# Kernel tuning notes

Measured on AMD Instinct MI355X. Metric: run time of the kernel, lower is better.

Reference implementation:

```python
import jax, jax.numpy as jnp
import numpy as np

D_MODEL = 2048
N_HEADS = 16
HEAD_DIM = D_MODEL // N_HEADS


def setup_inputs() -> dict:
    key = jax.random.key(0)
    ks = jax.random.split(key, 9)
    s = 0.02
    B, S = 4, 2048
    return {
        "x": jax.random.normal(ks[0], (B, S, D_MODEL), dtype=jnp.float32),
        "Wq": jax.random.normal(ks[1], (D_MODEL, D_MODEL), dtype=jnp.float32) * s,
        "bq": jnp.zeros((D_MODEL,), dtype=jnp.float32),
        "Wk": jax.random.normal(ks[2], (D_MODEL, D_MODEL), dtype=jnp.float32) * s,
        "bk": jnp.zeros((D_MODEL,), dtype=jnp.float32),
        "Wv": jax.random.normal(ks[3], (D_MODEL, D_MODEL), dtype=jnp.float32) * s,
        "bv": jnp.zeros((D_MODEL,), dtype=jnp.float32),
        "Wo": jax.random.normal(ks[4], (D_MODEL, D_MODEL), dtype=jnp.float32) * s,
        "bo": jnp.zeros((D_MODEL,), dtype=jnp.float32),
    }


def reference(x, Wq, bq, Wk, bk, Wv, bv, Wo, bo):
    B, S, _ = x.shape
    scale = jnp.asarray(np.sqrt(HEAD_DIM), dtype=x.dtype)

    def split_heads(t):  # [B,S,D] -> [B,H,S,hd]
        return t.reshape(B, S, N_HEADS, HEAD_DIM).transpose(0, 2, 1, 3)

    q = split_heads(x @ Wq + bq)
    k = split_heads(x @ Wk + bk)
    v = split_heads(x @ Wv + bv)

    # scores: [B,H,S,S]
    attn = jnp.einsum('bhqd,bhkd->bhqk', q, k) / scale
    kv_len = S
    causal = jnp.triu(jnp.ones((S, kv_len), dtype=bool), k=kv_len - S + 1)
    attn = jnp.where(causal[None, None], -jnp.inf, attn)
    attn = jax.nn.softmax(attn, axis=-1)
    # dropout is identity (p=0 / eval mode)
    out = jnp.einsum('bhqk,bhkd->bhqd', attn, v)
    out = out.transpose(0, 2, 1, 3).reshape(B, S, D_MODEL)
    return out @ Wo + bo
```

## Files before the change

### kernel.cpp

```cpp
#include <hip/hip_runtime.h>
#include <hip/hip_bf16.h>

#define DEV __device__ __forceinline__

typedef __bf16 bf16_t;
typedef __bf16 bf16x8 __attribute__((ext_vector_type(8)));
typedef __bf16 bf16x4 __attribute__((ext_vector_type(4)));
typedef float f32x4 __attribute__((ext_vector_type(4)));
typedef float f32x16 __attribute__((ext_vector_type(16)));
typedef unsigned int u32;
typedef unsigned short u16;
typedef u32 u32x4 __attribute__((ext_vector_type(4)));

constexpr int D_MODEL = 2048;
constexpr int SEQ = 2048;
constexpr int BATCH = 4;
constexpr int N_HEADS = 16;
constexpr int HEAD_DIM = 128;
constexpr int TOK = BATCH * SEQ;

DEV void gload_lds16(const void* g, void* l) {
  __builtin_amdgcn_global_load_lds(
      (const __attribute__((address_space(1))) unsigned int*)g,
      (__attribute__((address_space(3))) unsigned int*)l, 16, 0, 0);
}

DEV float fast_exp2(float x) {
#if __has_builtin(__builtin_amdgcn_exp2f)
  return __builtin_amdgcn_exp2f(x);
#else
  return exp2f(x);
#endif
}

DEV u32 pack2(float lo, float hi) {
  u16 a = __builtin_bit_cast(u16, (bf16_t)lo);
  u16 b = __builtin_bit_cast(u16, (bf16_t)hi);
  return (u32)a | ((u32)b << 16);
}

#define MFMA16(a, b, c) __builtin_amdgcn_mfma_f32_16x16x32_bf16((a), (b), (c), 0, 0, 0)
#define MFMA32(a, b, c) __builtin_amdgcn_mfma_f32_32x32x16_bf16((a), (b), (c), 0, 0, 0)

__global__ void k_prep(const float* __restrict__ x, bf16_t* __restrict__ xb,
                       const float* __restrict__ Wq, const float* __restrict__ Wk,
                       const float* __restrict__ Wv, const float* __restrict__ Wo,
                       bf16_t* __restrict__ WqkvT, bf16_t* __restrict__ WoT) {
  const int z = blockIdx.z;
  if (z < 4) {
    __shared__ float t[32][33];
    const float* W = z == 0 ? Wq : z == 1 ? Wk : z == 2 ? Wv : Wo;
    bf16_t* Wt = z < 3 ? WqkvT + (size_t)z * D_MODEL * D_MODEL : WoT;
    int k0 = blockIdx.x * 32, n0 = blockIdx.y * 32;
    int tx = threadIdx.x, ty = threadIdx.y;
#pragma unroll
    for (int r = ty; r < 32; r += 8)
      t[r][tx] = W[(size_t)(k0 + r) * D_MODEL + n0 + tx];
    __syncthreads();
#pragma unroll
    for (int r = ty; r < 32; r += 8)
      Wt[(size_t)(n0 + r) * D_MODEL + k0 + tx] = (bf16_t)t[tx][r];
  } else {
    const int n4 = TOK * D_MODEL / 4;
    const int tid = threadIdx.y * 32 + threadIdx.x;
    int i = (blockIdx.y * 64 + blockIdx.x) * 256 + tid;
    const int stride = 64 * 64 * 256;
    for (; i < n4; i += stride) {
      float4 v = ((const float4*)x)[i];
      bf16x4 o;
      o[0] = (bf16_t)v.x; o[1] = (bf16_t)v.y; o[2] = (bf16_t)v.z; o[3] = (bf16_t)v.w;
      ((bf16x4*)xb)[i] = o;
    }
  }
}

template <int MODE>
__global__ __launch_bounds__(512, 2) void k_gemm256(const bf16_t* __restrict__ A,
                                                    const bf16_t* __restrict__ Bt,
                                                    const float* __restrict__ b0p,
                                                    const float* __restrict__ b1p,
                                                    const float* __restrict__ b2p,
                                                    void* __restrict__ o0,
                                                    void* __restrict__ o1,
                                                    void* __restrict__ o2) {
  constexpr int K = D_MODEL;
  constexpr int NTOT = (MODE == 0) ? 3 * D_MODEL : D_MODEL;
  constexpr int NT = K / 64;
  constexpr int NBM = TOK / 256;
  __shared__ __attribute__((aligned(16))) bf16_t sh[2][2][2][8192];

  const int bid = blockIdx.x;
  const int cpx = gridDim.x >> 3;
  const int swz = (bid & 7) * cpx + (bid >> 3);
  const int grp = swz / (NBM * 4);
  const int rem = swz % (NBM * 4);
  const int bm = rem >> 2;
  const int bn = grp * 4 + (rem & 3);

  const int tid = threadIdx.x;
  const int lane = tid & 63;
  const int w = tid >> 6;
  const int wm = w >> 2, wn = w & 3;
  const int lr = lane & 15, lg = lane >> 4;

  const bf16_t* Agl[2];
  const bf16_t* Bgl[2];
  int ldsg[2];
#pragma unroll
  for (int l = 0; l < 2; ++l) {
    int g = l * 512 + tid;
    int r = g >> 2, c = g & 3;
    int csw = c ^ ((r ^ (r >> 2)) & 3);
    Agl[l] = A + (size_t)(bm * 256 + r) * K + csw * 8;
    Bgl[l] = Bt + (size_t)(bn * 256 + r) * K + csw * 8;
    ldsg[l] = g * 8;
  }

  auto SA = [&](int buf, int t, int kh) {
    const int off = t * 64 + kh * 32;
#pragma unroll
    for (int l = 0; l < 2; ++l) gload_lds16(Agl[l] + off, &sh[buf][0][kh][ldsg[l]]);
  };
  auto SB = [&](int buf, int t, int kh) {
    const int off = t * 64 + kh * 32;
#pragma unroll
    for (int l = 0; l < 2; ++l) gload_lds16(Bgl[l] + off, &sh[buf][1][kh][ldsg[l]]);
  };

  int offA[8], offB[4];
  const int cx = lg ^ ((lr ^ (lr >> 2)) & 3);
#pragma unroll
  for (int i = 0; i < 8; ++i) offA[i] = (wm * 128 + i * 16 + lr) * 32 + cx * 8;
#pragma unroll
  for (int j = 0; j < 4; ++j) offB[j] = (wn * 64 + j * 16 + lr) * 32 + cx * 8;

  f32x4 acc[8][4] = {};
  bf16x8 af[8], bf_[4];

  SA(0, 0, 0); SB(0, 0, 0); SA(0, 0, 1); SB(0, 0, 1);

#define MFMA_ROW(i)                                  \
  acc[i][0] = MFMA16(af[i], bf_[0], acc[i][0]);      \
  acc[i][1] = MFMA16(af[i], bf_[1], acc[i][1]);      \
  acc[i][2] = MFMA16(af[i], bf_[2], acc[i][2]);      \
  acc[i][3] = MFMA16(af[i], bf_[3], acc[i][3]);

  for (int t = 0; t < NT; ++t) {
    const int cur = t & 1, nxt = cur ^ 1;
    const int t1 = (t + 1 < NT) ? t + 1 : NT - 1;
#pragma unroll
    for (int kh = 0; kh < 2; ++kh) {
      asm volatile("s_waitcnt vmcnt(4)" ::: "memory");
      __builtin_amdgcn_s_barrier();
#pragma unroll
      for (int j = 0; j < 4; ++j) bf_[j] = *(const bf16x8*)&sh[cur][1][kh][offB[j]];
#pragma unroll
      for (int i = 0; i < 8; ++i) af[i] = *(const bf16x8*)&sh[cur][0][kh][offA[i]];
      SA(nxt, t1, kh);
      SB(nxt, t1, kh);
      __builtin_amdgcn_s_setprio(1);
      asm volatile("s_waitcnt lgkmcnt(6)" ::: "memory");
      __builtin_amdgcn_sched_barrier(0);
      MFMA_ROW(0) MFMA_ROW(1)
      asm volatile("s_waitcnt lgkmcnt(4)" ::: "memory");
      __builtin_amdgcn_sched_barrier(0);
      MFMA_ROW(2) MFMA_ROW(3)
      asm volatile("s_waitcnt lgkmcnt(2)" ::: "memory");
      __builtin_amdgcn_sched_barrier(0);
      MFMA_ROW(4) MFMA_ROW(5)
      asm volatile("s_waitcnt lgkmcnt(0)" ::: "memory");
      __builtin_amdgcn_sched_barrier(0);
      MFMA_ROW(6) MFMA_ROW(7)
      __builtin_amdgcn_s_setprio(0);
    }
  }
#undef MFMA_ROW

  asm volatile("s_waitcnt vmcnt(0) lgkmcnt(0)" ::: "memory");

#pragma unroll
  for (int i = 0; i < 8; ++i) {
    const int row = bm * 256 + wm * 128 + i * 16 + lg * 4;
#pragma unroll
    for (int jn = 0; jn < 4; ++jn) {
      const int col = bn * 256 + wn * 64 + jn * 16 + lr;
      if (MODE == 1) {
        const float bv = b0p[col];
        float* Cf = (float*)o0;
#pragma unroll
        for (int j = 0; j < 4; ++j)
          Cf[(size_t)(row + j) * D_MODEL + col] = acc[i][jn][j] + bv;
      } else {
        const int sel = col >> 11, cl = col & 2047;
        const float bv = (sel == 0 ? b0p : sel == 1 ? b1p : b2p)[cl];
        if (sel < 2) {
          bf16_t* dst = (bf16_t*)(sel == 0 ? o0 : o1);
#pragma unroll
          for (int j = 0; j < 4; ++j)
            dst[(size_t)(row + j) * D_MODEL + cl] = (bf16_t)(acc[i][jn][j] + bv);
        } else {
          const int bb2 = row >> 11, s = row & 2047;
          bf16x4 ov;
#pragma unroll
          for (int j = 0; j < 4; ++j) ov[j] = (bf16_t)(acc[i][jn][j] + bv);
          bf16_t* Vt = (bf16_t*)o2;
          *(bf16x4*)(Vt + (((size_t)(bb2 * 16 + (cl >> 7))) * 128 + (cl & 127)) * 2048 + s) = ov;
        }
      }
    }
  }
}

__global__ __launch_bounds__(256, 3) void k_attn(const bf16_t* __restrict__ Q,
                                                 const bf16_t* __restrict__ K,
                                                 const bf16_t* __restrict__ Vt,
                                                 bf16_t* __restrict__ AO) {
  const int fid = blockIdx.x;
  const int qb = 15 - (fid >> 6);
  const int bh = fid & 63;
  const int b = bh >> 4, h = bh & 15;
  const int w = threadIdx.x >> 6, lane = threadIdx.x & 63;
  const int l31 = lane & 31, hl = lane >> 5;
  const int nt = 4 * qb + 4;

  __shared__ __attribute__((aligned(16))) bf16_t Ks[2][32 * 128];
  __shared__ __attribute__((aligned(16))) bf16_t Vs[2][128 * 32];

  const bf16_t* kbase = K + (size_t)(b * SEQ) * D_MODEL + h * HEAD_DIM;
  const bf16_t* vtbase = Vt + (size_t)bh * HEAD_DIM * SEQ;
  const float C = 0.12751949848078418f;

  auto STAGE = [&](int buf, int kt) {
    const int tt = threadIdx.x;
#pragma unroll
    for (int p = 0; p < 2; ++p) {
      int g = p * 256 + tt;
      int r = g >> 4, c = g & 15;
      gload_lds16(kbase + (size_t)(kt * 32 + r) * D_MODEL + ((c ^ (r & 7)) * 8),
                  &Ks[buf][(size_t)(g & ~63) * 8]);
    }
#pragma unroll
    for (int p = 0; p < 2; ++p) {
      int g = p * 256 + tt;
      int r = g >> 2, c = g & 3;
      gload_lds16(vtbase + (size_t)r * SEQ + kt * 32 + ((c ^ ((r ^ (r >> 2)) & 3)) * 8),
                  &Vs[buf][(size_t)(g & ~63) * 8]);
    }
  };

  const int qw0 = qb * 128 + w * 32;
  const int qa = qw0 + l31;

  const bf16_t* qp = Q + (size_t)(b * SEQ + qa) * D_MODEL + h * HEAD_DIM + hl * 8;
  bf16x8 qf[8];
#pragma unroll
  for (int step = 0; step < 8; ++step) qf[step] = *(const bf16x8*)(qp + step * 16);

  f32x16 oacc[4];
#pragma unroll
  for (int db = 0; db < 4; ++db)
#pragma unroll
    for (int r = 0; r < 16; ++r) oacc[db][r] = 0.f;
  float m = -1e30f, lsum = 0.f;

  STAGE(0, 0);
  asm volatile("s_waitcnt vmcnt(0)" ::: "memory");
  __syncthreads();

  int buf = 0;
  for (int kt = 0; kt < nt; ++kt) {
    if (kt + 1 < nt) STAGE(buf ^ 1, kt + 1);

    if (kt * 32 < qw0 + 32) {
      f32x16 sacc;
#pragma unroll
      for (int r = 0; r < 16; ++r) sacc[r] = 0.f;
      const bf16_t* kr = &Ks[buf][l31 * 128];
      const int rx = l31 & 7;
      __builtin_amdgcn_s_setprio(1);
#pragma unroll
      for (int step = 0; step < 8; ++step) {
        bf16x8 kf = *(const bf16x8*)(kr + (((step * 2 + hl) ^ rx) * 8));
        sacc = MFMA32(kf, qf[step], sacc);
      }
      __builtin_amdgcn_s_setprio(0);

      const bool domask = (kt * 32 + 31 > qw0);
#pragma unroll
      for (int r = 0; r < 16; ++r) {
        float v = sacc[r] * C;
        if (domask) {
          int kv = kt * 32 + 4 * hl + (r & 3) + 8 * (r >> 2);
          if (kv > qa) v = -1e30f;
        }
        sacc[r] = v;
      }
      float mx8[8];
#pragma unroll
      for (int r = 0; r < 8; ++r) mx8[r] = fmaxf(sacc[r], sacc[r + 8]);
#pragma unroll
      for (int r = 0; r < 4; ++r) mx8[r] = fmaxf(mx8[r], mx8[r + 4]);
      float tm = fmaxf(fmaxf(mx8[0], mx8[1]), fmaxf(mx8[2], mx8[3]));
      tm = fmaxf(tm, __shfl_xor(tm, 32));

      if (!__all(tm <= m + 11.5f)) {
        const float mn = fmaxf(m, tm);
        const float al = fast_exp2(m - mn);
        lsum *= al;
#pragma unroll
        for (int db = 0; db < 4; ++db)
#pragma unroll
          for (int r = 0; r < 16; ++r) oacc[db][r] *= al;
        m = mn;
      }

#pragma unroll
      for (int r = 0; r < 16; ++r) sacc[r] = fast_exp2(sacc[r] - m);
      float sm8[8];
#pragma unroll
      for (int r = 0; r < 8; ++r) sm8[r] = sacc[r] + sacc[r + 8];
#pragma unroll
      for (int r = 0; r < 4; ++r) sm8[r] = sm8[r] + sm8[r + 4];
      float ls = (sm8[0] + sm8[1]) + (sm8[2] + sm8[3]);
      lsum += ls + __shfl_xor(ls, 32);

      bf16x8 pb[2];
#pragma unroll
      for (int ck = 0; ck < 2; ++ck) {
        u32 a0 = pack2(sacc[8 * ck + 0], sacc[8 * ck + 1]);
        u32 a1 = pack2(sacc[8 * ck + 2], sacc[8 * ck + 3]);
        u32 b0 = pack2(sacc[8 * ck + 4], sacc[8 * ck + 5]);
        u32 b1 = pack2(sacc[8 * ck + 6], sacc[8 * ck + 7]);
        u32 send0 = hl ? a0 : b0, send1 = hl ? a1 : b1;
        u32 keep0 = hl ? b0 : a0, keep1 = hl ? b1 : a1;
        u32 r0 = __shfl_xor(send0, 32), r1 = __shfl_xor(send1, 32);
        u32x4 fv;
        fv[0] = hl ? r0 : keep0;
        fv[1] = hl ? r1 : keep1;
        fv[2] = hl ? keep0 : r0;
        fv[3] = hl ? keep1 : r1;
        pb[ck] = __builtin_bit_cast(bf16x8, fv);
      }

      __builtin_amdgcn_s_setprio(1);
#pragma unroll
      for (int db = 0; db < 4; ++db) {
        const int vrow = db * 32 + l31;
        const bf16_t* vr = &Vs[buf][vrow * 32];
        const int vx = (vrow ^ (vrow >> 2)) & 3;
#pragma unroll
        for (int ck = 0; ck < 2; ++ck) {
          bf16x8 vf = *(const bf16x8*)(vr + (((ck * 2 + hl) ^ vx) * 8));
          oacc[db] = MFMA32(vf, pb[ck], oacc[db]);
        }
      }
      __builtin_amdgcn_s_setprio(0);
    }

    __syncthreads();
    buf ^= 1;
  }

  const float inv = 1.f / lsum;
  bf16_t* ao = AO + (size_t)(b * SEQ + qa) * D_MODEL + h * HEAD_DIM;
#pragma unroll
  for (int db = 0; db < 4; ++db)
#pragma unroll
    for (int g = 0; g < 4; ++g) {
      bf16x4 ov;
#pragma unroll
      for (int j = 0; j < 4; ++j) ov[j] = (bf16_t)(oacc[db][4 * g + j] * inv);
      *(bf16x4*)(ao + db * 32 + 8 * g + 4 * hl) = ov;
    }
}

extern "C" void kernel_launch(void* const* d_in, const int* in_sizes, int n_in,
                              void* d_out, int out_size, void* d_ws, size_t ws_size,
                              hipStream_t stream) {
  const float* x  = (const float*)d_in[0];
  const float* Wq = (const float*)d_in[1];
  const float* bq = (const float*)d_in[2];
  const float* Wk = (const float*)d_in[3];
  const float* bk = (const float*)d_in[4];
  const float* Wv = (const float*)d_in[5];
  const float* bv = (const float*)d_in[6];
  const float* Wo = (const float*)d_in[7];
  const float* bo = (const float*)d_in[8];

  const size_t SZ_X = (size_t)TOK * D_MODEL * sizeof(bf16_t);
  const size_t SZ_W = (size_t)D_MODEL * D_MODEL * sizeof(bf16_t);

  char* p = (char*)d_ws;
  bf16_t* xb    = (bf16_t*)p;                     p += SZ_X;
  bf16_t* WqkvT = (bf16_t*)p;                     p += 3 * SZ_W;
  bf16_t* WoT   = (bf16_t*)p;                     p += SZ_W;
  bf16_t* Qm    = (bf16_t*)p;                     p += SZ_X;
  bf16_t* Km    = (bf16_t*)p;                     p += SZ_X;
  bf16_t* Vt    = (bf16_t*)p;                     p += SZ_X;
  bf16_t* AO    = xb;

  k_prep<<<dim3(64, 64, 5), dim3(32, 8), 0, stream>>>(x, xb, Wq, Wk, Wv, Wo, WqkvT, WoT);

  const int gqkv = (TOK / 256) * (3 * D_MODEL / 256);
  k_gemm256<0><<<gqkv, 512, 0, stream>>>(xb, WqkvT, bq, bk, bv, Qm, Km, Vt);

  k_attn<<<1024, 256, 0, stream>>>(Qm, Km, Vt, AO);

  const int go = (TOK / 256) * (D_MODEL / 256);
  k_gemm256<1><<<go, 512, 0, stream>>>(AO, WoT, bo, nullptr, nullptr, d_out, nullptr, nullptr);
}
```

Measured before the change: 415.6 us.

## Triple-buffer attention K/V staging and simplify GEMM to single-K-slice double buffering

The attention kernel moves from double to triple buffering of K/V tiles. It prefetches two tiles ahead, waits with a partial vmcnt, and uses one barrier per iteration instead of a trailing __syncthreads. The GEMM kernel drops its split 64-wide K step with per-half prefetch in favour of 32-wide K tiles, where each step fully drains vmcnt(0) before the barrier. This halves GEMM shared memory but exposes global load latency in the GEMM, since loads are issued only one step ahead and fully waited on.

```diff
diff --git a/kernel.cpp b/kernel.cpp
--- a/kernel.cpp
+++ b/kernel.cpp
@@ -85,9 +85,9 @@
                                                     void* __restrict__ o2) {
   constexpr int K = D_MODEL;
   constexpr int NTOT = (MODE == 0) ? 3 * D_MODEL : D_MODEL;
-  constexpr int NT = K / 64;
+  constexpr int NT = K / 32;
   constexpr int NBM = TOK / 256;
-  __shared__ __attribute__((aligned(16))) bf16_t sh[2][2][2][8192];
+  __shared__ __attribute__((aligned(16))) bf16_t sh[2][2][8192];
 
   const int bid = blockIdx.x;
   const int cpx = gridDim.x >> 3;
@@ -116,15 +116,15 @@
     ldsg[l] = g * 8;
   }
 
-  auto SA = [&](int buf, int t, int kh) {
-    const int off = t * 64 + kh * 32;
-#pragma unroll
-    for (int l = 0; l < 2; ++l) gload_lds16(Agl[l] + off, &sh[buf][0][kh][ldsg[l]]);
+  auto SA = [&](int buf, int t) {
+    const int off = t * 32;
+#pragma unroll
+    for (int l = 0; l < 2; ++l) gload_lds16(Agl[l] + off, &sh[buf][0][ldsg[l]]);
   };
-  auto SB = [&](int buf, int t, int kh) {
-    const int off = t * 64 + kh * 32;
-#pragma unroll
-    for (int l = 0; l < 2; ++l) gload_lds16(Bgl[l] + off, &sh[buf][1][kh][ldsg[l]]);
+  auto SB = [&](int buf, int t) {
+    const int off = t * 32;
+#pragma unroll
+    for (int l = 0; l < 2; ++l) gload_lds16(Bgl[l] + off, &sh[buf][1][ldsg[l]]);
   };
 
   int offA[8], offB[4];
@@ -137,7 +137,7 @@
   f32x4 acc[8][4] = {};
   bf16x8 af[8], bf_[4];
 
-  SA(0, 0, 0); SB(0, 0, 0); SA(0, 0, 1); SB(0, 0, 1);
+  SA(0, 0); SB(0, 0);
 
 #define MFMA_ROW(i)                                  \
   acc[i][0] = MFMA16(af[i], bf_[0], acc[i][0]);      \
@@ -147,32 +147,28 @@
 
   for (int t = 0; t < NT; ++t) {
     const int cur = t & 1, nxt = cur ^ 1;
-    const int t1 = (t + 1 < NT) ? t + 1 : NT - 1;
-#pragma unroll
-    for (int kh = 0; kh < 2; ++kh) {
-      asm volatile("s_waitcnt vmcnt(4)" ::: "memory");
-      __builtin_amdgcn_s_barrier();
-#pragma unroll
-      for (int j = 0; j < 4; ++j) bf_[j] = *(const bf16x8*)&sh[cur][1][kh][offB[j]];
-#pragma unroll
-      for (int i = 0; i < 8; ++i) af[i] = *(const bf16x8*)&sh[cur][0][kh][offA[i]];
-      SA(nxt, t1, kh);
-      SB(nxt, t1, kh);
-      __builtin_amdgcn_s_setprio(1);
-      asm volatile("s_waitcnt lgkmcnt(6)" ::: "memory");
-      __builtin_amdgcn_sched_barrier(0);
-      MFMA_ROW(0) MFMA_ROW(1)
-      asm volatile("s_waitcnt lgkmcnt(4)" ::: "memory");
-      __builtin_amdgcn_sched_barrier(0);
-      MFMA_ROW(2) MFMA_ROW(3)
-      asm volatile("s_waitcnt lgkmcnt(2)" ::: "memory");
-      __builtin_amdgcn_sched_barrier(0);
-      MFMA_ROW(4) MFMA_ROW(5)
-      asm volatile("s_waitcnt lgkmcnt(0)" ::: "memory");
-      __builtin_amdgcn_sched_barrier(0);
-      MFMA_ROW(6) MFMA_ROW(7)
-      __builtin_amdgcn_s_setprio(0);
-    }
+    asm volatile("s_waitcnt vmcnt(0)" ::: "memory");
+    __builtin_amdgcn_s_barrier();
+    asm volatile("" ::: "memory");
+    if (t + 1 < NT) { SA(nxt, t + 1); SB(nxt, t + 1); }
+#pragma unroll
+    for (int j = 0; j < 4; ++j) bf_[j] = *(const bf16x8*)&sh[cur][1][offB[j]];
+#pragma unroll
+    for (int i = 0; i < 8; ++i) af[i] = *(const bf16x8*)&sh[cur][0][offA[i]];
+    __builtin_amdgcn_s_setprio(1);
+    asm volatile("s_waitcnt lgkmcnt(6)" ::: "memory");
+    __builtin_amdgcn_sched_barrier(0);
+    MFMA_ROW(0) MFMA_ROW(1)
+    asm volatile("s_waitcnt lgkmcnt(4)" ::: "memory");
+    __builtin_amdgcn_sched_barrier(0);
+    MFMA_ROW(2) MFMA_ROW(3)
+    asm volatile("s_waitcnt lgkmcnt(2)" ::: "memory");
+    __builtin_amdgcn_sched_barrier(0);
+    MFMA_ROW(4) MFMA_ROW(5)
+    asm volatile("s_waitcnt lgkmcnt(0)" ::: "memory");
+    __builtin_amdgcn_sched_barrier(0);
+    MFMA_ROW(6) MFMA_ROW(7)
+    __builtin_amdgcn_s_setprio(0);
   }
 #undef MFMA_ROW
 
@@ -223,8 +219,8 @@
   const int l31 = lane & 31, hl = lane >> 5;
   const int nt = 4 * qb + 4;
 
-  __shared__ __attribute__((aligned(16))) bf16_t Ks[2][32 * 128];
-  __shared__ __attribute__((aligned(16))) bf16_t Vs[2][128 * 32];
+  __shared__ __attribute__((aligned(16))) bf16_t Ks[3][32 * 128];
+  __shared__ __attribute__((aligned(16))) bf16_t Vs[3][128 * 32];
 
   const bf16_t* kbase = K + (size_t)(b * SEQ) * D_MODEL + h * HEAD_DIM;
   const bf16_t* vtbase = Vt + (size_t)bh * HEAD_DIM * SEQ;
@@ -264,18 +260,24 @@
   float m = -1e30f, lsum = 0.f;
 
   STAGE(0, 0);
-  asm volatile("s_waitcnt vmcnt(0)" ::: "memory");
-  __syncthreads();
-
-  int buf = 0;
+  STAGE(1, 1);
+
+  int cur = 0, stg = 2;
   for (int kt = 0; kt < nt; ++kt) {
-    if (kt + 1 < nt) STAGE(buf ^ 1, kt + 1);
+    if (kt < nt - 1) {
+      asm volatile("s_waitcnt vmcnt(4)" ::: "memory");
+    } else {
+      asm volatile("s_waitcnt vmcnt(0)" ::: "memory");
+    }
+    __builtin_amdgcn_s_barrier();
+    asm volatile("" ::: "memory");
+    if (kt + 2 < nt) STAGE(stg, kt + 2);
 
     if (kt * 32 < qw0 + 32) {
       f32x16 sacc;
 #pragma unroll
       for (int r = 0; r < 16; ++r) sacc[r] = 0.f;
-      const bf16_t* kr = &Ks[buf][l31 * 128];
+      const bf16_t* kr = &Ks[cur][l31 * 128];
       const int rx = l31 & 7;
       __builtin_amdgcn_s_setprio(1);
 #pragma unroll
@@ -346,7 +348,7 @@
 #pragma unroll
       for (int db = 0; db < 4; ++db) {
         const int vrow = db * 32 + l31;
-        const bf16_t* vr = &Vs[buf][vrow * 32];
+        const bf16_t* vr = &Vs[cur][vrow * 32];
         const int vx = (vrow ^ (vrow >> 2)) & 3;
 #pragma unroll
         for (int ck = 0; ck < 2; ++ck) {
@@ -357,8 +359,8 @@
       __builtin_amdgcn_s_setprio(0);
     }
 
-    __syncthreads();
-    buf ^= 1;
+    cur = (cur == 2) ? 0 : cur + 1;
+    stg = (stg == 2) ? 0 : stg + 1;
   }
 
   const float inv = 1.f / lsum;
```

After: 427.4 us. 2.8% more time.
